# Kernel tuning notes

Hardware: AMD Instinct MI355X
Metric: run time of the kernel (lower is better)

## Reference

```python
import math
import jax, jax.numpy as jnp
import numpy as np

B, L, C, H = 2, 2048, 1024, 16
D = C // H


def new_gelu(x):
    return 0.5 * x * (1.0 + jnp.tanh(math.sqrt(2.0 / math.pi) * (x + 0.044715 * x ** 3)))


def layer_norm(x, w, b, eps=1e-5):
    mu = jnp.mean(x, axis=-1, keepdims=True)
    var = jnp.var(x, axis=-1, keepdims=True)
    return (x - mu) * jax.lax.rsqrt(var + eps) * w + b


def setup_inputs() -> dict:
    key = jax.random.key(0)
    ks = jax.random.split(key, 8)
    s = 0.02
    return {
        "x": jax.random.normal(ks[0], (B, L, C), dtype=jnp.float32),
        "ln1_w": jnp.ones((C,), jnp.float32),
        "ln1_b": jnp.zeros((C,), jnp.float32),
        "w_attn": jax.random.normal(ks[1], (C, 3 * C), dtype=jnp.float32) * s,
        "b_attn": jnp.zeros((3 * C,), jnp.float32),
        "w_proj": jax.random.normal(ks[2], (C, C), dtype=jnp.float32) * s,
        "b_proj": jnp.zeros((C,), jnp.float32),
        "ln2_w": jnp.ones((C,), jnp.float32),
        "ln2_b": jnp.zeros((C,), jnp.float32),
        "w_fc": jax.random.normal(ks[3], (C, 4 * C), dtype=jnp.float32) * s,
        "b_fc": jnp.zeros((4 * C,), jnp.float32),
        "w_fc2": jax.random.normal(ks[4], (4 * C, C), dtype=jnp.float32) * s,
        "b_fc2": jnp.zeros((C,), jnp.float32),
    }


def reference(x, ln1_w, ln1_b, w_attn, b_attn, w_proj, b_proj,
              ln2_w, ln2_b, w_fc, b_fc, w_fc2, b_fc2):
    # --- self-attention sublayer (pre-LN) ---
    h = layer_norm(x, ln1_w, ln1_b)
    qkv = h @ w_attn + b_attn                              # [B, L, 3C]
    q, k, v = jnp.split(qkv, 3, axis=-1)
    q = q.reshape(B, L, H, D)
    k = k.reshape(B, L, H, D)
    v = v.reshape(B, L, H, D)
    att = jnp.einsum("bqhd,bkhd->bhqk", q, k) * (1.0 / math.sqrt(D))
    causal = jnp.tril(jnp.ones((L, L), dtype=bool))
    att = jnp.where(causal[None, None], att, -jnp.inf)
    att = jax.nn.softmax(att, axis=-1)
    y = jnp.einsum("bhqk,bkhd->bqhd", att, v).reshape(B, L, C)
    y = y @ w_proj + b_proj
    x = x + y
    # --- MLP sublayer (pre-LN) ---
    h = layer_norm(x, ln2_w, ln2_b)
    h = new_gelu(h @ w_fc + b_fc)
    h = h @ w_fc2 + b_fc2
    return x + h
```

## Files before the change

kernel.cpp:

```cpp
#include <hip/hip_runtime.h>
#include <math.h>

#define B_ 2
#define L_ 2048
#define C_ 1024
#define H_ 16
#define M_ (B_*L_)

typedef short s16x8 __attribute__((ext_vector_type(8)));
typedef float f32x4 __attribute__((ext_vector_type(4)));

__device__ __forceinline__ unsigned short f2bf(float f) {
    unsigned int u = __float_as_uint(f);
    u += 0x7fffu + ((u >> 16) & 1u);
    return (unsigned short)(u >> 16);
}

__device__ __forceinline__ float fexp2(float x) {
#if __has_builtin(__builtin_amdgcn_exp2f)
    return __builtin_amdgcn_exp2f(x);
#else
    return exp2f(x);
#endif
}

__device__ __forceinline__ float frcp(float x) {
#if __has_builtin(__builtin_amdgcn_rcpf)
    return __builtin_amdgcn_rcpf(x);
#else
    return 1.0f / x;
#endif
}

__device__ __forceinline__ void gl_lds16(const void* g, void* l) {
    __builtin_amdgcn_global_load_lds(
        (const __attribute__((address_space(1))) void*)g,
        (__attribute__((address_space(3))) void*)l, 16, 0, 0);
}

#define VMCNT8() asm volatile("s_waitcnt vmcnt(8)" ::: "memory")
#define VMCNT6() asm volatile("s_waitcnt vmcnt(6)" ::: "memory")
#define VMCNT0() asm volatile("s_waitcnt vmcnt(0)" ::: "memory")
#define LGKM0()  asm volatile("s_waitcnt lgkmcnt(0)" ::: "memory")

__device__ __forceinline__ void ln_row(const float* __restrict__ x,
                                       const float* __restrict__ w,
                                       const float* __restrict__ b,
                                       unsigned short* __restrict__ out,
                                       int row, int t,
                                       float* red0, float* red1, float* mv) {
    float4 v = ((const float4*)(x + (size_t)row * C_))[t];
    float s  = v.x + v.y + v.z + v.w;
    float s2 = v.x*v.x + v.y*v.y + v.z*v.z + v.w*v.w;
    #pragma unroll
    for (int off = 32; off > 0; off >>= 1) {
        s  += __shfl_down(s, off);
        s2 += __shfl_down(s2, off);
    }
    int wave = t >> 6, lane = t & 63;
    if (lane == 0) { red0[wave] = s; red1[wave] = s2; }
    __syncthreads();
    if (t == 0) {
        float a = red0[0] + red0[1] + red0[2] + red0[3];
        float c = red1[0] + red1[1] + red1[2] + red1[3];
        float mean = a * (1.0f / C_);
        mv[0] = mean;
        mv[1] = rsqrtf(c * (1.0f / C_) - mean * mean + 1e-5f);
    }
    __syncthreads();
    float mean = mv[0], rstd = mv[1];
    float4 wv = ((const float4*)w)[t];
    float4 bv = ((const float4*)b)[t];
    ushort4 o;
    o.x = f2bf((v.x - mean) * rstd * wv.x + bv.x);
    o.y = f2bf((v.y - mean) * rstd * wv.y + bv.y);
    o.z = f2bf((v.z - mean) * rstd * wv.z + bv.z);
    o.w = f2bf((v.w - mean) * rstd * wv.w + bv.w);
    *(ushort4*)&out[(size_t)row * C_ + t * 4] = o;
}

__global__ __launch_bounds__(256) void ln_bf16(const float* __restrict__ x,
                                               const float* __restrict__ w,
                                               const float* __restrict__ b,
                                               unsigned short* __restrict__ out) {
    __shared__ float red0[4], red1[4], mv[2];
    ln_row(x, w, b, out, blockIdx.x, threadIdx.x, red0, red1, mv);
}

__global__ __launch_bounds__(256) void prep_kernel(
    const float* __restrict__ W0, unsigned short* __restrict__ T0,
    const float* __restrict__ W1, unsigned short* __restrict__ T1,
    const float* __restrict__ W2, unsigned short* __restrict__ T2,
    const float* __restrict__ W3, unsigned short* __restrict__ T3,
    const float* __restrict__ x, const float* __restrict__ lnw,
    const float* __restrict__ lnb, unsigned short* __restrict__ h) {
    __shared__ unsigned short Ts[32][33];
    __shared__ float red0[4], red1[4], mv[2];
    int id = blockIdx.x;
    int t = threadIdx.x;
    if (id >= 12288) {
        ln_row(x, lnw, lnb, h, id - 12288, t, red0, red1, mv);
        return;
    }
    const float* W; unsigned short* WT; int R, C, bx, by;
    if (id < 3072)      { W = W0; WT = T0; R = 1024; C = 3072; bx = id % 96;  by = id / 96; }
    else if (id < 4096) { W = W1; WT = T1; R = 1024; C = 1024; id -= 3072; bx = id & 31;  by = id >> 5; }
    else if (id < 8192) { W = W2; WT = T2; R = 1024; C = 4096; id -= 4096; bx = id & 127; by = id >> 7; }
    else                { W = W3; WT = T3; R = 4096; C = 1024; id -= 8192; bx = id & 31;  by = id >> 5; }
    int tx = t & 31, ty = t >> 5;
    int c0 = bx * 32, r0 = by * 32;
    #pragma unroll
    for (int k = 0; k < 4; ++k)
        Ts[ty + 8*k][tx] = f2bf(W[(size_t)(r0 + ty + 8*k) * C + c0 + tx]);
    __syncthreads();
    #pragma unroll
    for (int k = 0; k < 4; ++k)
        WT[(size_t)(c0 + ty + 8*k) * R + r0 + tx] = Ts[tx][ty + 8*k];
}

__device__ __forceinline__ float gelu_f(float x) {
    float u2 = 1.5957691216057308f * (x + 0.044715f * x * x * x);
    return x * frcp(1.0f + __expf(-u2));
}

template<int ACT, int OBF, int TN, int SC, int KS, int VT, int XS>
__global__ __launch_bounds__(256) void bgemm(const unsigned short* __restrict__ A,
                                             const unsigned short* __restrict__ BT,
                                             const float* __restrict__ bias,
                                             const float* __restrict__ res,
                                             void* __restrict__ Cout,
                                             unsigned short* __restrict__ VtP,
                                             int M, int N, int K) {
    __shared__ __align__(16) unsigned short As[128 * 64];
    __shared__ __align__(16) unsigned short Bs[TN * 64];
    const int t = threadIdx.x, w = t >> 6, quad = (t & 63) >> 4, ln15 = t & 15;
    constexpr int FJ = TN / 32;
    const int woff_m = (w >> 1) * 64, woff_n = (w & 1) * (TN / 2);
    int bxi = blockIdx.x, byi = blockIdx.y;
    if (XS) {
        int id = bxi + (int)gridDim.x * byi;
        int nt = (int)gridDim.x, xcd = id & 7, loc = id >> 3;
        int per = (nt + 7) >> 3;
        bxi = xcd * per + (loc % per);
        byi = loc / per;
        if (bxi >= nt) { bxi = id % nt; byi = id / nt; }
    }
    const int m0g = byi * 128, n0g = bxi * TN;
    f32x4 acc[4][FJ];
    #pragma unroll
    for (int fi = 0; fi < 4; ++fi)
        #pragma unroll
        for (int fj = 0; fj < FJ; ++fj)
            #pragma unroll
            for (int i = 0; i < 4; ++i) acc[fi][fj][i] = 0.0f;

    const int kbeg = (KS > 1) ? (int)blockIdx.z * (K / KS) : 0;
    const int kiters = ((KS > 1) ? K / KS : K) >> 6;

    const unsigned short* ap[4];
    #pragma unroll
    for (int j = 0; j < 4; ++j) {
        int c = j * 256 + t, row = c >> 3, u = (c & 7) ^ (row & 7);
        ap[j] = A + (size_t)(m0g + row) * K + kbeg + u * 8;
    }
    const unsigned short* bp[FJ];
    #pragma unroll
    for (int j = 0; j < FJ; ++j) {
        int c = j * 256 + t, row = c >> 3, u = (c & 7) ^ (row & 7);
        bp[j] = BT + (size_t)(n0g + row) * K + kbeg + u * 8;
    }

    for (int kk = 0; kk < kiters; ++kk) {
        __syncthreads();
        #pragma unroll
        for (int j = 0; j < 4; ++j) {
            gl_lds16(ap[j], As + (j * 256 + w * 64) * 8);
            ap[j] += 64;
        }
        #pragma unroll
        for (int j = 0; j < FJ; ++j) {
            gl_lds16(bp[j], Bs + (j * 256 + w * 64) * 8);
            bp[j] += 64;
        }
        __syncthreads();
        #pragma unroll
        for (int s = 0; s < 2; ++s) {
            s16x8 af[4], bfr[FJ];
            #pragma unroll
            for (int f = 0; f < 4; ++f) {
                int row = woff_m + f * 16 + ln15;
                af[f] = *(const s16x8*)&As[(row * 8 + ((s * 4 + quad) ^ (row & 7))) * 8];
            }
            #pragma unroll
            for (int f = 0; f < FJ; ++f) {
                int row = woff_n + f * 16 + ln15;
                bfr[f] = *(const s16x8*)&Bs[(row * 8 + ((s * 4 + quad) ^ (row & 7))) * 8];
            }
            #pragma unroll
            for (int fi = 0; fi < 4; ++fi)
                #pragma unroll
                for (int fj = 0; fj < FJ; ++fj)
                    acc[fi][fj] = __builtin_amdgcn_mfma_f32_16x16x32_bf16(af[fi], bfr[fj], acc[fi][fj], 0, 0, 0);
        }
    }

    const int colb = n0g + woff_n + ln15;
    if (KS > 1) {
        float* P = (float*)Cout + (size_t)blockIdx.z * M * N;
        #pragma unroll
        for (int fj = 0; fj < FJ; ++fj) {
            const int col = colb + fj * 16;
            #pragma unroll
            for (int fi = 0; fi < 4; ++fi) {
                const int row0 = m0g + woff_m + fi * 16 + quad * 4;
                #pragma unroll
                for (int i = 0; i < 4; ++i)
                    P[(size_t)(row0 + i) * N + col] = acc[fi][fj][i];
            }
        }
        return;
    }
    #pragma unroll
    for (int fj = 0; fj < FJ; ++fj) {
        const int col = colb + fj * 16;
        const float bv = bias[col];
        const float sc = (SC && col < C_) ? 0.18033688011112042f : 1.0f;
        if (VT && col >= 2 * C_) {
            const int vcol = col - 2 * C_;
            #pragma unroll
            for (int fi = 0; fi < 4; ++fi) {
                const int row0 = m0g + woff_m + fi * 16 + quad * 4;
                const int bb = row0 >> 11, l = row0 & (L_ - 1);
                ushort4 pk;
                pk.x = f2bf(acc[fi][fj][0] + bv);
                pk.y = f2bf(acc[fi][fj][1] + bv);
                pk.z = f2bf(acc[fi][fj][2] + bv);
                pk.w = f2bf(acc[fi][fj][3] + bv);
                *(ushort4*)&VtP[(size_t)(bb * 1024 + vcol) * L_ + l] = pk;
            }
        } else {
            #pragma unroll
            for (int fi = 0; fi < 4; ++fi) {
                const int row0 = m0g + woff_m + fi * 16 + quad * 4;
                #pragma unroll
                for (int i = 0; i < 4; ++i) {
                    float v = acc[fi][fj][i] + bv;
                    if (ACT) v = gelu_f(v);
                    if (SC) v *= sc;
                    size_t off = (size_t)(row0 + i) * N + col;
                    if (res != nullptr) v += res[off];
                    if (OBF) ((unsigned short*)Cout)[off] = f2bf(v);
                    else     ((float*)Cout)[off] = v;
                }
            }
        }
    }
}

template<int ACT, int OBF, int BM, int SC, int KS, int VT, int XS>
__global__ __launch_bounds__(512) void bgemm2(const unsigned short* __restrict__ A,
                                              const unsigned short* __restrict__ BT,
                                              const float* __restrict__ bias,
                                              const float* __restrict__ res,
                                              void* __restrict__ Cout,
                                              unsigned short* __restrict__ VtP,
                                              int M, int N, int K) {
    constexpr int MR = BM / 32;
    constexpr int NR = 4;
    constexpr int WM = BM / 2;
    constexpr int RA = BM / 64;
    constexpr int RB = 4;
    __shared__ __align__(16) unsigned short As[2 * BM * 64];
    __shared__ __align__(16) unsigned short Bs[2 * 256 * 64];
    const int t = threadIdx.x, wv = t >> 6, quad = (t & 63) >> 4, ln15 = t & 15;
    const int wm = wv >> 2, wn = wv & 3;
    int bxi = blockIdx.x, byi = blockIdx.y;
    if (XS) {
        int id = bxi + (int)gridDim.x * byi;
        int nt = (int)gridDim.x, xcd = id & 7, loc = id >> 3;
        int per = nt >> 3;
        bxi = xcd * per + (loc % per);
        byi = loc / per;
    }
    const int m0g = byi * BM, n0g = bxi * 256;

    f32x4 acc[MR][NR];
    #pragma unroll
    for (int mr = 0; mr < MR; ++mr)
        #pragma unroll
        for (int nr = 0; nr < NR; ++nr)
            #pragma unroll
            for (int i = 0; i < 4; ++i) acc[mr][nr][i] = 0.0f;

    const int kbeg = (KS > 1) ? (int)blockIdx.z * (K / KS) : 0;
    const int NT = ((KS > 1) ? K / KS : K) >> 6;

    const unsigned short* ap[RA];
    #pragma unroll
    for (int j = 0; j < RA; ++j) {
        int c = j * 512 + t, row = c >> 3, u = (t & 7) ^ (row & 7);
        ap[j] = A + (size_t)(m0g + row) * K + kbeg + u * 8;
    }
    const unsigned short* bp[RB];
    #pragma unroll
    for (int j = 0; j < RB; ++j) {
        int c = j * 512 + t, row = c >> 3, u = (t & 7) ^ (row & 7);
        bp[j] = BT + (size_t)(n0g + row) * K + kbeg + u * 8;
    }

    auto STAGE = [&](int kt, int buf) {
        unsigned short* Ad = As + buf * (BM * 64);
        unsigned short* Bd = Bs + buf * (256 * 64);
        #pragma unroll
        for (int j = 0; j < RA; ++j)
            gl_lds16(ap[j] + (size_t)kt * 64, Ad + (j * 512 + wv * 64) * 8);
        #pragma unroll
        for (int j = 0; j < RB; ++j)
            gl_lds16(bp[j] + (size_t)kt * 64, Bd + (j * 512 + wv * 64) * 8);
    };

    STAGE(0, 0);
    STAGE(1, 1);
    if constexpr (RA + RB == 8) VMCNT8(); else VMCNT6();
    __builtin_amdgcn_s_barrier();

    int buf = 0;
    for (int kt = 0; kt < NT; ++kt) {
        const unsigned short* Ab = As + buf * (BM * 64);
        const unsigned short* Bb = Bs + buf * (256 * 64);
        s16x8 a0[MR], b0[NR], a1[MR], b1[NR];
        #pragma unroll
        for (int mr = 0; mr < MR; ++mr) {
            int row = wm * WM + mr * 16 + ln15;
            a0[mr] = *(const s16x8*)&Ab[(row * 8 + (quad ^ (row & 7))) * 8];
        }
        #pragma unroll
        for (int nr = 0; nr < NR; ++nr) {
            int row = wn * 64 + nr * 16 + ln15;
            b0[nr] = *(const s16x8*)&Bb[(row * 8 + (quad ^ (row & 7))) * 8];
        }
        #pragma unroll
        for (int mr = 0; mr < MR; ++mr)
            #pragma unroll
            for (int nr = 0; nr < NR; ++nr)
                acc[mr][nr] = __builtin_amdgcn_mfma_f32_16x16x32_bf16(a0[mr], b0[nr], acc[mr][nr], 0, 0, 0);
        #pragma unroll
        for (int mr = 0; mr < MR; ++mr) {
            int row = wm * WM + mr * 16 + ln15;
            a1[mr] = *(const s16x8*)&Ab[(row * 8 + ((4 + quad) ^ (row & 7))) * 8];
        }
        #pragma unroll
        for (int nr = 0; nr < NR; ++nr) {
            int row = wn * 64 + nr * 16 + ln15;
            b1[nr] = *(const s16x8*)&Bb[(row * 8 + ((4 + quad) ^ (row & 7))) * 8];
        }
        LGKM0();
        __builtin_amdgcn_sched_barrier(0);
        __builtin_amdgcn_s_barrier();
        if (kt + 2 < NT) STAGE(kt + 2, buf);
        __builtin_amdgcn_s_setprio(1);
        #pragma unroll
        for (int mr = 0; mr < MR; ++mr)
            #pragma unroll
            for (int nr = 0; nr < NR; ++nr)
                acc[mr][nr] = __builtin_amdgcn_mfma_f32_16x16x32_bf16(a1[mr], b1[nr], acc[mr][nr], 0, 0, 0);
        __builtin_amdgcn_s_setprio(0);
        if (kt + 2 < NT) {
            if constexpr (RA + RB == 8) VMCNT8(); else VMCNT6();
            __builtin_amdgcn_s_barrier();
        } else if (kt + 1 < NT) {
            VMCNT0();
            __builtin_amdgcn_s_barrier();
        }
        buf ^= 1;
    }

    const int colb = n0g + wn * 64 + ln15;
    if (KS > 1) {
        float* P = (float*)Cout + (size_t)blockIdx.z * M * N;
        #pragma unroll
        for (int nr = 0; nr < NR; ++nr) {
            const int col = colb + nr * 16;
            #pragma unroll
            for (int mr = 0; mr < MR; ++mr) {
                const int row0 = m0g + wm * WM + mr * 16 + quad * 4;
                #pragma unroll
                for (int i = 0; i < 4; ++i)
                    P[(size_t)(row0 + i) * N + col] = acc[mr][nr][i];
            }
        }
        return;
    }
    #pragma unroll
    for (int nr = 0; nr < NR; ++nr) {
        const int col = colb + nr * 16;
        const float bv = bias[col];
        const float sc = (SC && col < C_) ? 0.18033688011112042f : 1.0f;
        if (VT && col >= 2 * C_) {
            const int vcol = col - 2 * C_;
            #pragma unroll
            for (int mr = 0; mr < MR; ++mr) {
                const int row0 = m0g + wm * WM + mr * 16 + quad * 4;
                const int bb = row0 >> 11, l = row0 & (L_ - 1);
                ushort4 pk;
                pk.x = f2bf(acc[mr][nr][0] + bv);
                pk.y = f2bf(acc[mr][nr][1] + bv);
                pk.z = f2bf(acc[mr][nr][2] + bv);
                pk.w = f2bf(acc[mr][nr][3] + bv);
                *(ushort4*)&VtP[(size_t)(bb * 1024 + vcol) * L_ + l] = pk;
            }
        } else {
            #pragma unroll
            for (int mr = 0; mr < MR; ++mr) {
                const int row0 = m0g + wm * WM + mr * 16 + quad * 4;
                #pragma unroll
                for (int i = 0; i < 4; ++i) {
                    float v = acc[mr][nr][i] + bv;
                    if (ACT) v = gelu_f(v);
                    if (SC) v *= sc;
                    size_t off = (size_t)(row0 + i) * N + col;
                    if (res != nullptr) v += res[off];
                    if (OBF) ((unsigned short*)Cout)[off] = f2bf(v);
                    else     ((float*)Cout)[off] = v;
                }
            }
        }
    }
}

__global__ __launch_bounds__(256) void combine_out(const float* __restrict__ p,
                                                   const float* __restrict__ bias,
                                                   const float* __restrict__ res,
                                                   float* __restrict__ out) {
    int idx = blockIdx.x * 256 + threadIdx.x;
    size_t off = (size_t)idx * 4;
    float4 a = *(const float4*)&p[off];
    float4 b = *(const float4*)&p[(size_t)M_ * C_ + off];
    float4 r = *(const float4*)&res[off];
    float4 bb = *(const float4*)&bias[off & (C_ - 1)];
    float4 o;
    o.x = a.x + b.x + r.x + bb.x;
    o.y = a.y + b.y + r.y + bb.y;
    o.z = a.z + b.z + r.z + bb.z;
    o.w = a.w + b.w + r.w + bb.w;
    *(float4*)&out[off] = o;
}

__global__ __launch_bounds__(256) void attn_kernel(const unsigned short* __restrict__ qkv,
                                                   const unsigned short* __restrict__ Vt,
                                                   unsigned short* __restrict__ y) {
    __shared__ __align__(16) unsigned short Qs[64 * 64];
    __shared__ __align__(16) unsigned short Ks[128 * 64];
    __shared__ __align__(16) unsigned short Vs[64 * 128];
    const int t = threadIdx.x, w = t >> 6, quad = (t & 63) >> 4, ln15 = t & 15;
    const int wq = w >> 1, wk = w & 1;
    const int id = blockIdx.x;
    const int bh = (id & 7) * 4 + ((id >> 3) & 3);
    const int qpair = id >> 5;
    const int b = bh >> 4, h = bh & 15;

    #pragma unroll 1
    for (int rep = 0; rep < 2; ++rep) {
        const int qt = rep == 0 ? (31 - qpair) : qpair;
        const int q0 = qt * 64;
        if (rep) __syncthreads();
        #pragma unroll
        for (int j = 0; j < 2; ++j) {
            int c = j * 256 + t;
            int row = c >> 3, u = (c & 7) ^ (row & 7);
            gl_lds16(qkv + (size_t)(b * L_ + q0 + row) * (3*C_) + h * 64 + u * 8,
                     Qs + (j * 256 + w * 64) * 8);
        }
        __syncthreads();
        s16x8 qb[2][2];
        #pragma unroll
        for (int qf = 0; qf < 2; ++qf) {
            int row = wq * 32 + qf * 16 + ln15;
            #pragma unroll
            for (int s = 0; s < 2; ++s)
                qb[qf][s] = *(const s16x8*)&Qs[row * 64 + (((s * 4 + quad)) ^ (row & 7)) * 8];
        }

        f32x4 O[4][2];
        float m_[2] = {-INFINITY, -INFINITY}, l_[2] = {0.0f, 0.0f};
        #pragma unroll
        for (int df = 0; df < 4; ++df)
            #pragma unroll
            for (int qf = 0; qf < 2; ++qf)
                #pragma unroll
                for (int i = 0; i < 4; ++i) O[df][qf][i] = 0.0f;

        const int nkt = (qt >> 1) + 1;
        for (int kt = 0; kt < nkt; ++kt) {
            __syncthreads();
            #pragma unroll
            for (int j = 0; j < 4; ++j) {
                int c = j * 256 + t;
                int row = c >> 3, u = (c & 7) ^ (row & 7);
                gl_lds16(qkv + (size_t)(b * L_ + kt * 128 + row) * (3*C_) + C_ + h * 64 + u * 8,
                         Ks + (j * 256 + w * 64) * 8);
            }
            #pragma unroll
            for (int j = 0; j < 4; ++j) {
                int c = j * 256 + t;
                int row = c >> 4, u = (c & 15) ^ (row & 15);
                gl_lds16(Vt + (size_t)(bh * 64 + row) * L_ + kt * 128 + u * 8,
                         Vs + (j * 256 + w * 64) * 8);
            }
            __syncthreads();

            f32x4 St[2][4];
            #pragma unroll
            for (int qf = 0; qf < 2; ++qf)
                #pragma unroll
                for (int kf = 0; kf < 4; ++kf)
                    #pragma unroll
                    for (int i = 0; i < 4; ++i) St[qf][kf][i] = 0.0f;
            #pragma unroll
            for (int s = 0; s < 2; ++s) {
                s16x8 ka[4];
                #pragma unroll
                for (int kf = 0; kf < 4; ++kf) {
                    int row = wk * 64 + kf * 16 + ln15;
                    ka[kf] = *(const s16x8*)&Ks[row * 64 + ((s * 4 + quad) ^ (row & 7)) * 8];
                }
                #pragma unroll
                for (int qf = 0; qf < 2; ++qf)
                    #pragma unroll
                    for (int kf = 0; kf < 4; ++kf)
                        St[qf][kf] = __builtin_amdgcn_mfma_f32_16x16x32_bf16(ka[kf], qb[qf][s], St[qf][kf], 0, 0, 0);
            }
            __syncthreads();

            unsigned short* Pw = Ks + w * 2048;
            const bool diag = (kt == nkt - 1);
            #pragma unroll
            for (int qf = 0; qf < 2; ++qf) {
                const int qg = q0 + wq * 32 + qf * 16 + ln15;
                float mt = -INFINITY;
                if (diag) {
                    #pragma unroll
                    for (int kf = 0; kf < 4; ++kf)
                        #pragma unroll
                        for (int i = 0; i < 4; ++i) {
                            int key = kt * 128 + wk * 64 + kf * 16 + quad * 4 + i;
                            float sv = St[qf][kf][i];
                            sv = (key > qg) ? -INFINITY : sv;
                            St[qf][kf][i] = sv;
                            mt = fmaxf(mt, sv);
                        }
                } else {
                    #pragma unroll
                    for (int kf = 0; kf < 4; ++kf)
                        #pragma unroll
                        for (int i = 0; i < 4; ++i) mt = fmaxf(mt, St[qf][kf][i]);
                }
                mt = fmaxf(mt, __shfl_xor(mt, 16));
                mt = fmaxf(mt, __shfl_xor(mt, 32));
                const float mn = fmaxf(m_[qf], mt);
                const float ms = (mn == -INFINITY) ? 0.0f : mn;
                const float alpha = fexp2(m_[qf] - ms);
                float rs = 0.0f;
                #pragma unroll
                for (int kf = 0; kf < 4; ++kf)
                    #pragma unroll
                    for (int i = 0; i < 4; ++i) {
                        float e = fexp2(St[qf][kf][i] - ms);
                        St[qf][kf][i] = e;
                        rs += e;
                    }
                rs += __shfl_xor(rs, 16);
                rs += __shfl_xor(rs, 32);
                l_[qf] = l_[qf] * alpha + rs;
                m_[qf] = mn;
                #pragma unroll
                for (int df = 0; df < 4; ++df) O[df][qf] *= alpha;
                #pragma unroll
                for (int kf = 0; kf < 4; ++kf) {
                    int row = qf * 16 + ln15;
                    int slot = (kf * 2 + (quad >> 1)) ^ (row & 7);
                    unsigned u0 = __float_as_uint(St[qf][kf][0]) + 0x8000u;
                    unsigned u1 = __float_as_uint(St[qf][kf][1]) + 0x8000u;
                    unsigned u2 = __float_as_uint(St[qf][kf][2]) + 0x8000u;
                    unsigned u3 = __float_as_uint(St[qf][kf][3]) + 0x8000u;
                    uint2 pk;
                    pk.x = __builtin_amdgcn_perm(u1, u0, 0x07060302u);
                    pk.y = __builtin_amdgcn_perm(u3, u2, 0x07060302u);
                    *(uint2*)&Pw[row * 64 + slot * 8 + (quad & 1) * 4] = pk;
                }
            }

            #pragma unroll
            for (int s2 = 0; s2 < 2; ++s2) {
                s16x8 pb[2], va[4];
                #pragma unroll
                for (int qf = 0; qf < 2; ++qf) {
                    int row = qf * 16 + ln15;
                    pb[qf] = *(const s16x8*)&Pw[row * 64 + ((s2 * 4 + quad) ^ (row & 7)) * 8];
                }
                #pragma unroll
                for (int df = 0; df < 4; ++df) {
                    int row = df * 16 + ln15;
                    int uu = wk * 8 + s2 * 4 + quad;
                    va[df] = *(const s16x8*)&Vs[row * 128 + (uu ^ (row & 15)) * 8];
                }
                #pragma unroll
                for (int df = 0; df < 4; ++df)
                    #pragma unroll
                    for (int qf = 0; qf < 2; ++qf)
                        O[df][qf] = __builtin_amdgcn_mfma_f32_16x16x32_bf16(va[df], pb[qf], O[df][qf], 0, 0, 0);
            }
        }

        __syncthreads();
        float* OB  = (float*)Vs;
        float* MLm = (float*)Qs;
        float* MLl = MLm + 64;
        if (wk == 1) {
            #pragma unroll
            for (int qf = 0; qf < 2; ++qf) {
                int rq = wq * 32 + qf * 16 + ln15;
                if (quad == 0) { MLm[rq] = m_[qf]; MLl[rq] = l_[qf]; }
                #pragma unroll
                for (int df = 0; df < 4; ++df) {
                    float4 o;
                    o.x = O[df][qf][0]; o.y = O[df][qf][1]; o.z = O[df][qf][2]; o.w = O[df][qf][3];
                    *(float4*)&OB[rq * 64 + df * 16 + quad * 4] = o;
                }
            }
        }
        __syncthreads();
        if (wk == 0) {
            #pragma unroll
            for (int qf = 0; qf < 2; ++qf) {
                const int rq = wq * 32 + qf * 16 + ln15;
                const float m1 = MLm[rq], l1 = MLl[rq];
                const float mF = fmaxf(m_[qf], m1);
                float e0 = fexp2(m_[qf] - mF);
                float e1 = (m1 == -INFINITY) ? 0.0f : fexp2(m1 - mF);
                const float linv = frcp(l_[qf] * e0 + l1 * e1);
                e0 *= linv; e1 *= linv;
                #pragma unroll
                for (int df = 0; df < 4; ++df) {
                    float4 o1 = *(const float4*)&OB[rq * 64 + df * 16 + quad * 4];
                    ushort4 yv;
                    yv.x = f2bf(O[df][qf][0] * e0 + o1.x * e1);
                    yv.y = f2bf(O[df][qf][1] * e0 + o1.y * e1);
                    yv.z = f2bf(O[df][qf][2] * e0 + o1.z * e1);
                    yv.w = f2bf(O[df][qf][3] * e0 + o1.w * e1);
                    *(ushort4*)&y[(size_t)(b * L_ + q0 + rq) * C_ + h * 64 + df * 16 + quad * 4] = yv;
                }
            }
        }
    }
}

#define MB(x) ((size_t)(x) << 20)

extern "C" void kernel_launch(void* const* d_in, const int* in_sizes, int n_in,
                              void* d_out, int out_size, void* d_ws, size_t ws_size,
                              hipStream_t stream) {
    const float* x      = (const float*)d_in[0];
    const float* ln1_w  = (const float*)d_in[1];
    const float* ln1_b  = (const float*)d_in[2];
    const float* w_attn = (const float*)d_in[3];
    const float* b_attn = (const float*)d_in[4];
    const float* w_proj = (const float*)d_in[5];
    const float* b_proj = (const float*)d_in[6];
    const float* ln2_w  = (const float*)d_in[7];
    const float* ln2_b  = (const float*)d_in[8];
    const float* w_fc   = (const float*)d_in[9];
    const float* b_fc   = (const float*)d_in[10];
    const float* w_fc2  = (const float*)d_in[11];
    const float* b_fc2  = (const float*)d_in[12];
    float* out = (float*)d_out;

    char* ws = (char*)d_ws;
    unsigned short* wT1  = (unsigned short*)(ws + MB(0));
    unsigned short* wT2  = (unsigned short*)(ws + MB(6));
    unsigned short* wT3  = (unsigned short*)(ws + MB(8));
    unsigned short* wT4  = (unsigned short*)(ws + MB(16));
    unsigned short* h_bf = (unsigned short*)(ws + MB(24));
    unsigned short* qkv  = (unsigned short*)(ws + MB(32));
    unsigned short* Vt   = (unsigned short*)(ws + MB(56));
    unsigned short* y_bf = (unsigned short*)(ws + MB(64));
    float*          x1   = (float*)(ws + MB(72));
    unsigned short* f_bf = (unsigned short*)(ws + MB(88));
    float*          part = (float*)(ws + MB(32));
    dim3 b256(256), b512(512);

    prep_kernel<<<12288 + M_, b256, 0, stream>>>(w_attn, wT1, w_proj, wT2,
                                                 w_fc, wT3, w_fc2, wT4,
                                                 x, ln1_w, ln1_b, h_bf);
    bgemm<0,1,128,1,1,1,0><<<dim3(3*C_/128, M_/128), b256, 0, stream>>>(
        h_bf, wT1, b_attn, nullptr, qkv, Vt, M_, 3*C_, C_);
    attn_kernel<<<512, b256, 0, stream>>>(qkv, Vt, y_bf);
    bgemm<0,0,64,0,1,0,0><<<dim3(C_/64, M_/128), b256, 0, stream>>>(
        y_bf, wT2, b_proj, x, x1, nullptr, M_, C_, C_);
    ln_bf16<<<M_, b256, 0, stream>>>(x1, ln2_w, ln2_b, h_bf);
    bgemm2<1,1,256,0,1,0,1><<<dim3(4*C_/256, M_/256), b512, 0, stream>>>(
        h_bf, wT3, b_fc, nullptr, f_bf, nullptr, M_, 4*C_, C_);
    bgemm2<0,0,128,0,2,0,0><<<dim3(C_/256, M_/128, 2), b512, 0, stream>>>(
        f_bf, wT4, nullptr, nullptr, part, nullptr, M_, C_, 4*C_);
    combine_out<<<(M_*C_)/(4*256), b256, 0, stream>>>(part, b_fc2, x1, out);
}
```

Baseline: 336.6 us.

## Double-buffer K/V tiles in attention kernel to overlap loads with compute

The attention kernel now keeps two LDS buffers for K and V tiles, prefetching tile kt+1 while computing on tile kt, and replaces the per-iteration syncthreads with explicit waitcnt plus s_barrier. The first K/V tile is loaded alongside Q before the loop. The partial-output merge buffer also gets an XOR swizzle to reduce LDS bank conflicts. LDS use roughly doubles, which can lower occupancy, and the vmcnt(0) wait at the end of each iteration limits how much load latency is hidden.

New measurement: 334.1 us. About the same (-0.7%).

```diff
diff --git a/kernel.cpp b/kernel.cpp
--- a/kernel.cpp
+++ b/kernel.cpp
@@ -42,6 +42,7 @@
 #define VMCNT6() asm volatile("s_waitcnt vmcnt(6)" ::: "memory")
 #define VMCNT0() asm volatile("s_waitcnt vmcnt(0)" ::: "memory")
 #define LGKM0()  asm volatile("s_waitcnt lgkmcnt(0)" ::: "memory")
+#define SCHED0() __builtin_amdgcn_sched_barrier(0)
 
 __device__ __forceinline__ void ln_row(const float* __restrict__ x,
                                        const float* __restrict__ w,
@@ -450,8 +451,8 @@
                                                    const unsigned short* __restrict__ Vt,
                                                    unsigned short* __restrict__ y) {
     __shared__ __align__(16) unsigned short Qs[64 * 64];
-    __shared__ __align__(16) unsigned short Ks[128 * 64];
-    __shared__ __align__(16) unsigned short Vs[64 * 128];
+    __shared__ __align__(16) unsigned short Ks[2 * 128 * 64];
+    __shared__ __align__(16) unsigned short Vs[2 * 64 * 128];
     const int t = threadIdx.x, w = t >> 6, quad = (t & 63) >> 4, ln15 = t & 15;
     const int wq = w >> 1, wk = w & 1;
     const int id = blockIdx.x;
@@ -471,7 +472,22 @@
             gl_lds16(qkv + (size_t)(b * L_ + q0 + row) * (3*C_) + h * 64 + u * 8,
                      Qs + (j * 256 + w * 64) * 8);
         }
+        #pragma unroll
+        for (int j = 0; j < 4; ++j) {
+            int c = j * 256 + t;
+            int row = c >> 3, u = (c & 7) ^ (row & 7);
+            gl_lds16(qkv + (size_t)(b * L_ + row) * (3*C_) + C_ + h * 64 + u * 8,
+                     Ks + (j * 256 + w * 64) * 8);
+        }
+        #pragma unroll
+        for (int j = 0; j < 4; ++j) {
+            int c = j * 256 + t;
+            int row = c >> 4, u = (c & 15) ^ (row & 15);
+            gl_lds16(Vt + (size_t)(bh * 64 + row) * L_ + u * 8,
+                     Vs + (j * 256 + w * 64) * 8);
+        }
         __syncthreads();
+
         s16x8 qb[2][2];
         #pragma unroll
         for (int qf = 0; qf < 2; ++qf) {
@@ -491,23 +507,28 @@
                 for (int i = 0; i < 4; ++i) O[df][qf][i] = 0.0f;
 
         const int nkt = (qt >> 1) + 1;
+        int buf = 0;
         for (int kt = 0; kt < nkt; ++kt) {
-            __syncthreads();
-            #pragma unroll
-            for (int j = 0; j < 4; ++j) {
-                int c = j * 256 + t;
-                int row = c >> 3, u = (c & 7) ^ (row & 7);
-                gl_lds16(qkv + (size_t)(b * L_ + kt * 128 + row) * (3*C_) + C_ + h * 64 + u * 8,
-                         Ks + (j * 256 + w * 64) * 8);
-            }
-            #pragma unroll
-            for (int j = 0; j < 4; ++j) {
-                int c = j * 256 + t;
-                int row = c >> 4, u = (c & 15) ^ (row & 15);
-                gl_lds16(Vt + (size_t)(bh * 64 + row) * L_ + kt * 128 + u * 8,
-                         Vs + (j * 256 + w * 64) * 8);
-            }
-            __syncthreads();
+            unsigned short* Kb = Ks + buf * (128 * 64);
+            unsigned short* Vb = Vs + buf * (64 * 128);
+            unsigned short* Kn = Ks + (buf ^ 1) * (128 * 64);
+            unsigned short* Vn = Vs + (buf ^ 1) * (64 * 128);
+            if (kt + 1 < nkt) {
+                #pragma unroll
+                for (int j = 0; j < 4; ++j) {
+                    int c = j * 256 + t;
+                    int row = c >> 3, u = (c & 7) ^ (row & 7);
+                    gl_lds16(qkv + (size_t)(b * L_ + (kt + 1) * 128 + row) * (3*C_) + C_ + h * 64 + u * 8,
+                             Kn + (j * 256 + w * 64) * 8);
+                }
+                #pragma unroll
+                for (int j = 0; j < 4; ++j) {
+                    int c = j * 256 + t;
+                    int row = c >> 4, u = (c & 15) ^ (row & 15);
+                    gl_lds16(Vt + (size_t)(bh * 64 + row) * L_ + (kt + 1) * 128 + u * 8,
+                             Vn + (j * 256 + w * 64) * 8);
+                }
+            }
 
             f32x4 St[2][4];
             #pragma unroll
@@ -522,7 +543,7 @@
                 #pragma unroll
                 for (int kf = 0; kf < 4; ++kf) {
                     int row = wk * 64 + kf * 16 + ln15;
-                    ka[kf] = *(const s16x8*)&Ks[row * 64 + ((s * 4 + quad) ^ (row & 7)) * 8];
+                    ka[kf] = *(const s16x8*)&Kb[row * 64 + ((s * 4 + quad) ^ (row & 7)) * 8];
                 }
                 #pragma unroll
                 for (int qf = 0; qf < 2; ++qf)
@@ -530,9 +551,11 @@
                     for (int kf = 0; kf < 4; ++kf)
                         St[qf][kf] = __builtin_amdgcn_mfma_f32_16x16x32_bf16(ka[kf], qb[qf][s], St[qf][kf], 0, 0, 0);
             }
-            __syncthreads();
-
-            unsigned short* Pw = Ks + w * 2048;
+            LGKM0(); SCHED0();
+            __builtin_amdgcn_s_barrier();
+            SCHED0();
+
+            unsigned short* Pw = Kb + w * 2048;
             const bool diag = (kt == nkt - 1);
             #pragma unroll
             for (int qf = 0; qf < 2; ++qf) {
@@ -602,7 +625,7 @@
                 for (int df = 0; df < 4; ++df) {
                     int row = df * 16 + ln15;
                     int uu = wk * 8 + s2 * 4 + quad;
-                    va[df] = *(const s16x8*)&Vs[row * 128 + (uu ^ (row & 15)) * 8];
+                    va[df] = *(const s16x8*)&Vb[row * 128 + (uu ^ (row & 15)) * 8];
                 }
                 #pragma unroll
                 for (int df = 0; df < 4; ++df)
@@ -610,10 +633,17 @@
                     for (int qf = 0; qf < 2; ++qf)
                         O[df][qf] = __builtin_amdgcn_mfma_f32_16x16x32_bf16(va[df], pb[qf], O[df][qf], 0, 0, 0);
             }
+
+            if (kt + 1 < nkt) {
+                LGKM0(); VMCNT0(); SCHED0();
+                __builtin_amdgcn_s_barrier();
+                SCHED0();
+            }
+            buf ^= 1;
         }
 
         __syncthreads();
-        float* OB  = (float*)Vs;
+        float* OB  = (float*)Ks;
         float* MLm = (float*)Qs;
         float* MLl = MLm + 64;
         if (wk == 1) {
@@ -625,7 +655,7 @@
                 for (int df = 0; df < 4; ++df) {
                     float4 o;
                     o.x = O[df][qf][0]; o.y = O[df][qf][1]; o.z = O[df][qf][2]; o.w = O[df][qf][3];
-                    *(float4*)&OB[rq * 64 + df * 16 + quad * 4] = o;
+                    *(float4*)&OB[rq * 64 + (((df * 4 + quad) ^ (rq & 15)) << 2)] = o;
                 }
             }
         }
@@ -642,7 +672,7 @@
                 e0 *= linv; e1 *= linv;
                 #pragma unroll
                 for (int df = 0; df < 4; ++df) {
-                    float4 o1 = *(const float4*)&OB[rq * 64 + df * 16 + quad * 4];
+                    float4 o1 = *(const float4*)&OB[rq * 64 + (((df * 4 + quad) ^ (rq & 15)) << 2)];
                     ushort4 yv;
                     yv.x = f2bf(O[df][qf][0] * e0 + o1.x * e1);
                     yv.y = f2bf(O[df][qf][1] * e0 + o1.y * e1);
```
